# Optimization experiments

Hardware: AMD Instinct MI355X
Metric: run time of the kernel (lower is better)

## Reference

```python
import jax, jax.numpy as jnp
import numpy as np

DIST_SCALE = 10000.0   # divisor in kernel()
KERNEL_EPS = 0.0001    # additive epsilon before reciprocal


def setup_inputs() -> dict:
    key = jax.random.key(0)
    k1, k2, k3 = jax.random.split(key, 3)
    batch, keysize, dict_size, categories = 4096, 512, 16384, 128
    x = jax.random.normal(k1, (batch, keysize), dtype=jnp.float32)
    # keras TruncatedNormal(mean=0, stddev=3) approximated by scaled normal
    keys = 3.0 * jax.random.normal(k2, (dict_size, keysize), dtype=jnp.float32)
    V = jax.random.normal(k3, (dict_size, categories), dtype=jnp.float32)
    return {"x": x, "keys": keys, "V": V}


def reference(x, keys, V):
    # sq_distance(keys, x): (dict_size, batch)
    sq = (
        jnp.sum(keys * keys, axis=1, keepdims=True)            # (D, 1)
        - 2.0 * jnp.einsum("dk,bk->db", keys, x)               # (D, B)
        + jnp.sum(x * x, axis=1)[None, :]                      # (1, B)
    )
    kern = 1.0 / (sq / DIST_SCALE + KERNEL_EPS)                # (D, B)
    KV = jnp.einsum("db,dc->bc", kern, V)                      # (B, C)
    # original: diag(1 / (KV @ ones)) @ KV  ==  row-normalize by row sum
    return KV / jnp.sum(KV, axis=1, keepdims=True)
```

## Files before the change

### kernel.cpp

```cpp
#include <hip/hip_runtime.h>

#define BATCH 4096
#define DICT  16384
#define KDIM  512
#define CAT   128
#define ND    16
#define DSLICE (DICT/ND)
#define DCH   128
#define BT    256

typedef __attribute__((ext_vector_type(4))) float          f32x4;
typedef __attribute__((ext_vector_type(8))) short          short8;
typedef __attribute__((ext_vector_type(8))) unsigned short ushort8;
typedef __attribute__((ext_vector_type(4))) int            intx4;

__device__ __forceinline__ unsigned short f2bf(float f) {
  unsigned int u = __float_as_uint(f);
  return (unsigned short)((u + 0x7fffu + ((u >> 16) & 1u)) >> 16);
}

__device__ __forceinline__ unsigned int cvtpk_bf16(float lo, float hi) {
  unsigned int r;
  asm volatile("v_cvt_pk_bf16_f32 %0, %1, %2" : "=v"(r) : "v"(lo), "v"(hi));
  return r;
}

#define AS1 __attribute__((address_space(1)))
#define AS3 __attribute__((address_space(3)))
__device__ __forceinline__ void gl_lds16(const void* g, void* l) {
  __builtin_amdgcn_global_load_lds((AS1 void*)(g), (AS3 void*)(l), 16, 0, 0);
}

template <int N>
__device__ __forceinline__ void waitv() {
  if constexpr (N == 0)       asm volatile("s_waitcnt vmcnt(0)" ::: "memory");
  else if constexpr (N == 12) asm volatile("s_waitcnt vmcnt(12)" ::: "memory");
  else                        asm volatile("s_waitcnt vmcnt(14)" ::: "memory");
  __builtin_amdgcn_sched_barrier(0);
}

#define MFMA16(a, b, c) __builtin_amdgcn_mfma_f32_16x16x32_bf16((a), (b), (c), 0, 0, 0)

__global__ void prep_rows(const float* __restrict__ in,
                          unsigned short* __restrict__ ob,
                          float* __restrict__ sums) {
  const int lane = threadIdx.x & 63, wv = threadIdx.x >> 6;
  const int row = blockIdx.x * 4 + wv;
  const float* rp = in + ((size_t)row << 9);
  float4 a = *(const float4*)(rp + lane * 8);
  float4 b = *(const float4*)(rp + lane * 8 + 4);
  float s = a.x*a.x + a.y*a.y + a.z*a.z + a.w*a.w
          + b.x*b.x + b.y*b.y + b.z*b.z + b.w*b.w;
  ushort8 o;
  o[0]=f2bf(a.x); o[1]=f2bf(a.y); o[2]=f2bf(a.z); o[3]=f2bf(a.w);
  o[4]=f2bf(b.x); o[5]=f2bf(b.y); o[6]=f2bf(b.z); o[7]=f2bf(b.w);
  *(ushort8*)(ob + ((size_t)row << 9) + lane * 8) = o;
  #pragma unroll
  for (int m = 32; m; m >>= 1) s += __shfl_xor(s, m);
  if (lane == 0) sums[row] = s;
}

__global__ void prep_vt(const float* __restrict__ V,
                        unsigned short* __restrict__ Vt) {
  __shared__ float t[64][129];
  const int d0 = blockIdx.x * 64;
  const int tid = threadIdx.x;
  #pragma unroll
  for (int j = 0; j < 32; ++j) {
    int idx = j * 256 + tid;
    t[idx >> 7][idx & 127] = V[((size_t)d0 << 7) + idx];
  }
  __syncthreads();
  #pragma unroll
  for (int j = 0; j < 32; ++j) {
    int idx = j * 256 + tid;
    int cc = idx >> 6, dd = idx & 63;
    int p = dd & 31, qq = p >> 3, jj = p & 7;
    int src = (dd & 32) + 4 * qq + ((jj < 4) ? jj : (12 + jj));
    Vt[((size_t)cc << 14) + d0 + dd] = f2bf(t[src][cc]);
  }
}

__global__ __launch_bounds__(256, 1)
void varkeys_fused(const unsigned short* __restrict__ xb,
                   const unsigned short* __restrict__ kb,
                   const unsigned short* __restrict__ vt,
                   const float* __restrict__ sx,
                   const float* __restrict__ sk,
                   float* __restrict__ kvp) {
  __shared__ __attribute__((aligned(16))) char lds[131072];
  char* const VsA = lds + 98304;
  char* const VsB = lds + 114688;

  const int tid  = threadIdx.x;
  const int lane = tid & 63;
  const int wv   = tid >> 6;
  const int c    = lane & 15;
  const int h    = lane >> 4;
  const int sw   = (lane & 7) << 4;
  const int l3   = lane >> 3;

  const int bid    = blockIdx.x;
  const int btile  = bid & 15;
  const int dslice = bid >> 4;
  const int b0     = btile * BT;
  const int dbase  = dslice * DSLICE;

  float sxv[4];
  #pragma unroll
  for (int fj = 0; fj < 4; ++fj) sxv[fj] = sx[b0 + wv * 64 + fj * 16 + c];

  const int rowS = wv * 8 + l3;
  const int ofs  = (((lane & 7) ^ l3) << 4);

  const char* xbB = (const char*)xb;
  const char* kbB = (const char*)kb;
  const char* vtB = (const char*)vt;

  const f32x4 zero = {0.f, 0.f, 0.f, 0.f};
  f32x4 acc[4][8];
  #pragma unroll
  for (int j = 0; j < 4; ++j)
    #pragma unroll
    for (int n = 0; n < 8; ++n) acc[j][n] = zero;

  auto stageAB = [&](int ns) {
    const int dg2 = dbase + (ns >> 3) * DCH;
    const int kb2 = (ns & 7) << 7;
    char* A2 = lds + (ns & 1) * 16384;
    char* B2 = lds + 32768 + (ns & 1) * 32768;
    #pragma unroll
    for (int cl = 0; cl < 4; ++cl)
      gl_lds16(kbB + ((size_t)(dg2 + cl * 32 + rowS) << 10) + kb2 + ofs,
               A2 + cl * 4096 + wv * 1024);
    #pragma unroll
    for (int cl = 0; cl < 8; ++cl)
      gl_lds16(xbB + ((size_t)(b0 + cl * 32 + rowS) << 10) + kb2 + ofs,
               B2 + cl * 4096 + wv * 1024);
  };

  stageAB(0);

  f32x4 skq[8];

  for (int dc = 0; dc < DSLICE / DCH; ++dc) {
    const int dg = dbase + dc * DCH;

    f32x4 S[8][4];
    #pragma unroll
    for (int i = 0; i < 8; ++i)
      #pragma unroll
      for (int fj = 0; fj < 4; ++fj) S[i][fj] = zero;

    #pragma unroll
    for (int kk = 0; kk < 8; ++kk) {
      __builtin_amdgcn_s_barrier();
      if (kk == 0) {
        #pragma unroll
        for (int i = 0; i < 8; ++i)
          skq[i] = *(const f32x4*)(sk + dg + i * 16 + h * 4);
      }
      const int ns = dc * 8 + kk + 1;
      if (ns < 64) stageAB(ns);
      if (kk >= 2 && kk <= 5) {
        char* const VsH = (kk < 4) ? VsA : VsB;
        const int hv = (kk < 4) ? 0 : 1;
        #pragma unroll
        for (int t = 0; t < 2; ++t) {
          const int cl = ((kk - 2) & 1) * 2 + t;
          gl_lds16(vtB + ((size_t)(cl * 32 + rowS) << 15)
                       + ((size_t)(dg + hv * 64) << 1) + ofs,
                   VsH + cl * 4096 + wv * 1024);
        }
      }
      if (ns == 64) waitv<0>();
      else if (kk >= 2 && kk <= 5) waitv<14>();
      else waitv<12>();
      __builtin_amdgcn_s_barrier();
      __builtin_amdgcn_sched_barrier(0);

      const char* As = lds + (kk & 1) * 16384;
      const char* Bs = lds + 32768 + (kk & 1) * 32768;
      #pragma unroll
      for (int kf = 0; kf < 2; ++kf) {
        const int ko = (kf * 64 + h * 16) ^ sw;
        short8 bf[4];
        #pragma unroll
        for (int fj = 0; fj < 4; ++fj)
          bf[fj] = *(const short8*)(Bs + ((wv * 64 + fj * 16 + c) << 7) + ko);
        #pragma unroll
        for (int i = 0; i < 8; ++i) {
          short8 af = *(const short8*)(As + ((i * 16 + c) << 7) + ko);
          #pragma unroll
          for (int fj = 0; fj < 4; ++fj)
            S[i][fj] = MFMA16(af, bf[fj], S[i][fj]);
        }
      }
    }

    #pragma unroll
    for (int hv = 0; hv < 2; ++hv) {
      const char* VsH = hv ? VsB : VsA;
      #pragma unroll
      for (int dkh = 0; dkh < 2; ++dkh) {
        const int dk = hv * 2 + dkh;
        short8 pa[4];
        #pragma unroll
        for (int fj = 0; fj < 4; ++fj) {
          const float sv = sxv[fj];
          const f32x4 sA = S[2 * dk][fj];
          const f32x4 sB = S[2 * dk + 1][fj];
          const f32x4 kA = skq[2 * dk];
          const f32x4 kB = skq[2 * dk + 1];
          float a0 = 10000.f * __builtin_amdgcn_rcpf(kA[0] + sv - 2.f * sA[0] + 1.f);
          float a1 = 10000.f * __builtin_amdgcn_rcpf(kA[1] + sv - 2.f * sA[1] + 1.f);
          float a2 = 10000.f * __builtin_amdgcn_rcpf(kA[2] + sv - 2.f * sA[2] + 1.f);
          float a3 = 10000.f * __builtin_amdgcn_rcpf(kA[3] + sv - 2.f * sA[3] + 1.f);
          float b0f = 10000.f * __builtin_amdgcn_rcpf(kB[0] + sv - 2.f * sB[0] + 1.f);
          float b1f = 10000.f * __builtin_amdgcn_rcpf(kB[1] + sv - 2.f * sB[1] + 1.f);
          float b2f = 10000.f * __builtin_amdgcn_rcpf(kB[2] + sv - 2.f * sB[2] + 1.f);
          float b3f = 10000.f * __builtin_amdgcn_rcpf(kB[3] + sv - 2.f * sB[3] + 1.f);
          intx4 fw;
          fw[0] = (int)cvtpk_bf16(a0, a1);
          fw[1] = (int)cvtpk_bf16(a2, a3);
          fw[2] = (int)cvtpk_bf16(b0f, b1f);
          fw[3] = (int)cvtpk_bf16(b2f, b3f);
          pa[fj] = *(short8*)&fw;
        }
        const int ko = (dkh * 64 + h * 16) ^ sw;
        #pragma unroll
        for (int fc = 0; fc < 8; ++fc) {
          short8 vb = *(const short8*)(VsH + ((fc * 16 + c) << 7) + ko);
          #pragma unroll
          for (int fj = 0; fj < 4; ++fj)
            acc[fj][fc] = MFMA16(pa[fj], vb, acc[fj][fc]);
        }
      }
    }
  }

  __syncthreads();
  float* eb = (float*)(lds + (wv << 15));
  #pragma unroll
  for (int fj = 0; fj < 4; ++fj)
    #pragma unroll
    for (int r = 0; r < 4; ++r) {
      const int brow = fj * 16 + h * 4 + r;
      #pragma unroll
      for (int fc = 0; fc < 8; ++fc)
        eb[(brow << 7) + fc * 16 + c] = acc[fj][fc][r];
    }
  __syncthreads();
  float* op = kvp + (((size_t)dslice * BATCH + b0) << 7);
  const float* ebase = (const float*)lds;
  #pragma unroll
  for (int t = 0; t < 32; ++t) {
    const int row = t * 8 + (tid >> 5);
    f32x4 v = *(const f32x4*)(ebase + (row << 7) + ((tid & 31) << 2));
    *(f32x4*)(op + (((size_t)row) << 7) + ((tid & 31) << 2)) = v;
  }
}

__global__ void reduce_norm(const float* __restrict__ part, float* __restrict__ out) {
  const int lane = threadIdx.x & 63, wv = threadIdx.x >> 6;
  const int b = blockIdx.x * 4 + wv;
  float v0 = 0.f, v1 = 0.f;
  #pragma unroll
  for (int s = 0; s < ND; ++s) {
    const float* p = part + ((((size_t)s << 12) + b) << 7);
    v0 += p[lane]; v1 += p[lane + 64];
  }
  float t = v0 + v1;
  #pragma unroll
  for (int m = 32; m; m >>= 1) t += __shfl_xor(t, m);
  out[((size_t)b << 7) + lane]      = v0 / t;
  out[((size_t)b << 7) + lane + 64] = v1 / t;
}

extern "C" void kernel_launch(void* const* d_in, const int* in_sizes, int n_in,
                              void* d_out, int out_size, void* d_ws, size_t ws_size,
                              hipStream_t stream) {
  (void)in_sizes; (void)n_in; (void)out_size; (void)ws_size;
  const float* x    = (const float*)d_in[0];
  const float* keys = (const float*)d_in[1];
  const float* V    = (const float*)d_in[2];
  float* out = (float*)d_out;
  char* ws = (char*)d_ws;
  unsigned short* xb = (unsigned short*)(ws);
  unsigned short* kb = (unsigned short*)(ws + ((size_t)4 << 20));
  unsigned short* vt = (unsigned short*)(ws + ((size_t)20 << 20));
  float* sx  = (float*)(ws + ((size_t)24 << 20));
  float* sk  = (float*)(ws + ((size_t)24 << 20) + (1 << 16));
  float* kvp = (float*)(ws + ((size_t)25 << 20));

  prep_rows<<<BATCH / 4, 256, 0, stream>>>(x, xb, sx);
  prep_rows<<<DICT / 4, 256, 0, stream>>>(keys, kb, sk);
  prep_vt<<<DICT / 64, 256, 0, stream>>>(V, vt);
  varkeys_fused<<<(BATCH / BT) * ND, 256, 0, stream>>>(xb, kb, vt, sx, sk, kvp);
  reduce_norm<<<BATCH / 4, 256, 0, stream>>>(kvp, out);
}
```

Before: 157.7 us.

## Split fused kernel across 8 waves with dict-half partitioning and LDS reduction

```diff
diff --git a/kernel.cpp b/kernel.cpp
--- a/kernel.cpp
+++ b/kernel.cpp
@@ -33,9 +33,9 @@
 
 template <int N>
 __device__ __forceinline__ void waitv() {
-  if constexpr (N == 0)       asm volatile("s_waitcnt vmcnt(0)" ::: "memory");
-  else if constexpr (N == 12) asm volatile("s_waitcnt vmcnt(12)" ::: "memory");
-  else                        asm volatile("s_waitcnt vmcnt(14)" ::: "memory");
+  if constexpr (N == 0)      asm volatile("s_waitcnt vmcnt(0)" ::: "memory");
+  else if constexpr (N == 6) asm volatile("s_waitcnt vmcnt(6)" ::: "memory");
+  else                       asm volatile("s_waitcnt vmcnt(7)" ::: "memory");
   __builtin_amdgcn_sched_barrier(0);
 }
 
@@ -81,7 +81,7 @@
   }
 }
 
-__global__ __launch_bounds__(256, 1)
+__global__ __launch_bounds__(512, 2)
 void varkeys_fused(const unsigned short* __restrict__ xb,
                    const unsigned short* __restrict__ kb,
                    const unsigned short* __restrict__ vt,
@@ -95,6 +95,8 @@
   const int tid  = threadIdx.x;
   const int lane = tid & 63;
   const int wv   = tid >> 6;
+  const int dw   = wv >> 2;
+  const int bw   = wv & 3;
   const int c    = lane & 15;
   const int h    = lane >> 4;
   const int sw   = (lane & 7) << 4;
@@ -108,9 +110,9 @@
 
   float sxv[4];
   #pragma unroll
-  for (int fj = 0; fj < 4; ++fj) sxv[fj] = sx[b0 + wv * 64 + fj * 16 + c];
-
-  const int rowS = wv * 8 + l3;
+  for (int fj = 0; fj < 4; ++fj) sxv[fj] = sx[b0 + bw * 64 + fj * 16 + c];
+
+  const int rowT = wv * 8 + l3;
   const int ofs  = (((lane & 7) ^ l3) << 4);
 
   const char* xbB = (const char*)xb;
@@ -130,52 +132,49 @@
     char* A2 = lds + (ns & 1) * 16384;
     char* B2 = lds + 32768 + (ns & 1) * 32768;
     #pragma unroll
+    for (int cl = 0; cl < 2; ++cl)
+      gl_lds16(kbB + ((size_t)(dg2 + cl * 64 + rowT) << 10) + kb2 + ofs,
+               A2 + cl * 8192 + wv * 1024);
+    #pragma unroll
     for (int cl = 0; cl < 4; ++cl)
-      gl_lds16(kbB + ((size_t)(dg2 + cl * 32 + rowS) << 10) + kb2 + ofs,
-               A2 + cl * 4096 + wv * 1024);
-    #pragma unroll
-    for (int cl = 0; cl < 8; ++cl)
-      gl_lds16(xbB + ((size_t)(b0 + cl * 32 + rowS) << 10) + kb2 + ofs,
-               B2 + cl * 4096 + wv * 1024);
+      gl_lds16(xbB + ((size_t)(b0 + cl * 64 + rowT) << 10) + kb2 + ofs,
+               B2 + cl * 8192 + wv * 1024);
   };
 
   stageAB(0);
 
-  f32x4 skq[8];
+  f32x4 skq[4];
 
   for (int dc = 0; dc < DSLICE / DCH; ++dc) {
     const int dg = dbase + dc * DCH;
 
-    f32x4 S[8][4];
-    #pragma unroll
-    for (int i = 0; i < 8; ++i)
+    f32x4 S[4][4];
+    #pragma unroll
+    for (int i = 0; i < 4; ++i)
       #pragma unroll
       for (int fj = 0; fj < 4; ++fj) S[i][fj] = zero;
 
     #pragma unroll
     for (int kk = 0; kk < 8; ++kk) {
       __builtin_amdgcn_s_barrier();
-      if (kk == 0) {
-        #pragma unroll
-        for (int i = 0; i < 8; ++i)
-          skq[i] = *(const f32x4*)(sk + dg + i * 16 + h * 4);
+      if (kk == 7) {
+        #pragma unroll
+        for (int i = 0; i < 4; ++i)
+          skq[i] = *(const f32x4*)(sk + dg + dw * 64 + i * 16 + h * 4);
       }
       const int ns = dc * 8 + kk + 1;
       if (ns < 64) stageAB(ns);
       if (kk >= 2 && kk <= 5) {
         char* const VsH = (kk < 4) ? VsA : VsB;
         const int hv = (kk < 4) ? 0 : 1;
-        #pragma unroll
-        for (int t = 0; t < 2; ++t) {
-          const int cl = ((kk - 2) & 1) * 2 + t;
-          gl_lds16(vtB + ((size_t)(cl * 32 + rowS) << 15)
-                       + ((size_t)(dg + hv * 64) << 1) + ofs,
-                   VsH + cl * 4096 + wv * 1024);
-        }
+        const int vcl = kk & 1;
+        gl_lds16(vtB + ((size_t)(vcl * 64 + rowT) << 15)
+                     + ((size_t)(dg + hv * 64) << 1) + ofs,
+                 VsH + vcl * 8192 + wv * 1024);
       }
       if (ns == 64) waitv<0>();
-      else if (kk >= 2 && kk <= 5) waitv<14>();
-      else waitv<12>();
+      else if (kk >= 2 && kk <= 5) waitv<7>();
+      else waitv<6>();
       __builtin_amdgcn_s_barrier();
       __builtin_amdgcn_sched_barrier(0);
 
@@ -187,10 +186,10 @@
         short8 bf[4];
         #pragma unroll
         for (int fj = 0; fj < 4; ++fj)
-          bf[fj] = *(const short8*)(Bs + ((wv * 64 + fj * 16 + c) << 7) + ko);
-        #pragma unroll
-        for (int i = 0; i < 8; ++i) {
-          short8 af = *(const short8*)(As + ((i * 16 + c) << 7) + ko);
+          bf[fj] = *(const short8*)(Bs + ((bw * 64 + fj * 16 + c) << 7) + ko);
+        #pragma unroll
+        for (int i = 0; i < 4; ++i) {
+          short8 af = *(const short8*)(As + ((dw * 64 + i * 16 + c) << 7) + ko);
           #pragma unroll
           for (int fj = 0; fj < 4; ++fj)
             S[i][fj] = MFMA16(af, bf[fj], S[i][fj]);
@@ -198,66 +197,70 @@
       }
     }
 
-    #pragma unroll
-    for (int hv = 0; hv < 2; ++hv) {
-      const char* VsH = hv ? VsB : VsA;
-      #pragma unroll
-      for (int dkh = 0; dkh < 2; ++dkh) {
-        const int dk = hv * 2 + dkh;
-        short8 pa[4];
-        #pragma unroll
-        for (int fj = 0; fj < 4; ++fj) {
-          const float sv = sxv[fj];
-          const f32x4 sA = S[2 * dk][fj];
-          const f32x4 sB = S[2 * dk + 1][fj];
-          const f32x4 kA = skq[2 * dk];
-          const f32x4 kB = skq[2 * dk + 1];
-          float a0 = 10000.f * __builtin_amdgcn_rcpf(kA[0] + sv - 2.f * sA[0] + 1.f);
-          float a1 = 10000.f * __builtin_amdgcn_rcpf(kA[1] + sv - 2.f * sA[1] + 1.f);
-          float a2 = 10000.f * __builtin_amdgcn_rcpf(kA[2] + sv - 2.f * sA[2] + 1.f);
-          float a3 = 10000.f * __builtin_amdgcn_rcpf(kA[3] + sv - 2.f * sA[3] + 1.f);
-          float b0f = 10000.f * __builtin_amdgcn_rcpf(kB[0] + sv - 2.f * sB[0] + 1.f);
-          float b1f = 10000.f * __builtin_amdgcn_rcpf(kB[1] + sv - 2.f * sB[1] + 1.f);
-          float b2f = 10000.f * __builtin_amdgcn_rcpf(kB[2] + sv - 2.f * sB[2] + 1.f);
-          float b3f = 10000.f * __builtin_amdgcn_rcpf(kB[3] + sv - 2.f * sB[3] + 1.f);
-          intx4 fw;
-          fw[0] = (int)cvtpk_bf16(a0, a1);
-          fw[1] = (int)cvtpk_bf16(a2, a3);
-          fw[2] = (int)cvtpk_bf16(b0f, b1f);
-          fw[3] = (int)cvtpk_bf16(b2f, b3f);
-          pa[fj] = *(short8*)&fw;
-        }
-        const int ko = (dkh * 64 + h * 16) ^ sw;
-        #pragma unroll
-        for (int fc = 0; fc < 8; ++fc) {
-          short8 vb = *(const short8*)(VsH + ((fc * 16 + c) << 7) + ko);
-          #pragma unroll
-          for (int fj = 0; fj < 4; ++fj)
-            acc[fj][fc] = MFMA16(pa[fj], vb, acc[fj][fc]);
-        }
+    const char* VsH = dw ? VsB : VsA;
+    #pragma unroll
+    for (int dkh = 0; dkh < 2; ++dkh) {
+      short8 pa[4];
+      #pragma unroll
+      for (int fj = 0; fj < 4; ++fj) {
+        const float sv = sxv[fj];
+        const f32x4 sA = S[2 * dkh][fj];
+        const f32x4 sB = S[2 * dkh + 1][fj];
+        const f32x4 kA = skq[2 * dkh];
+        const f32x4 kB = skq[2 * dkh + 1];
+        float a0 = 10000.f * __builtin_amdgcn_rcpf(kA[0] + sv - 2.f * sA[0] + 1.f);
+        float a1 = 10000.f * __builtin_amdgcn_rcpf(kA[1] + sv - 2.f * sA[1] + 1.f);
+        float a2 = 10000.f * __builtin_amdgcn_rcpf(kA[2] + sv - 2.f * sA[2] + 1.f);
+        float a3 = 10000.f * __builtin_amdgcn_rcpf(kA[3] + sv - 2.f * sA[3] + 1.f);
+        float b0f = 10000.f * __builtin_amdgcn_rcpf(kB[0] + sv - 2.f * sB[0] + 1.f);
+        float b1f = 10000.f * __builtin_amdgcn_rcpf(kB[1] + sv - 2.f * sB[1] + 1.f);
+        float b2f = 10000.f * __builtin_amdgcn_rcpf(kB[2] + sv - 2.f * sB[2] + 1.f);
+        float b3f = 10000.f * __builtin_amdgcn_rcpf(kB[3] + sv - 2.f * sB[3] + 1.f);
+        intx4 fw;
+        fw[0] = (int)cvtpk_bf16(a0, a1);
+        fw[1] = (int)cvtpk_bf16(a2, a3);
+        fw[2] = (int)cvtpk_bf16(b0f, b1f);
+        fw[3] = (int)cvtpk_bf16(b2f, b3f);
+        pa[fj] = *(short8*)&fw;
+      }
+      const int ko = (dkh * 64 + h * 16) ^ sw;
+      #pragma unroll
+      for (int fc = 0; fc < 8; ++fc) {
+        short8 vb = *(const short8*)(VsH + ((fc * 16 + c) << 7) + ko);
+        #pragma unroll
+        for (int fj = 0; fj < 4; ++fj)
+          acc[fj][fc] = MFMA16(pa[fj], vb, acc[fj][fc]);
       }
     }
   }
 
   __syncthreads();
-  float* eb = (float*)(lds + (wv << 15));
-  #pragma unroll
-  for (int fj = 0; fj < 4; ++fj)
-    #pragma unroll
-    for (int r = 0; r < 4; ++r) {
-      const int brow = fj * 16 + h * 4 + r;
+  if (dw == 1) {
+    #pragma unroll
+    for (int fj = 0; fj < 4; ++fj)
       #pragma unroll
       for (int fc = 0; fc < 8; ++fc)
-        eb[(brow << 7) + fc * 16 + c] = acc[fj][fc][r];
-    }
+        *(f32x4*)(lds + bw * 32768 + (fj * 8 + fc) * 1024 + lane * 16) = acc[fj][fc];
+  }
   __syncthreads();
-  float* op = kvp + (((size_t)dslice * BATCH + b0) << 7);
-  const float* ebase = (const float*)lds;
-  #pragma unroll
-  for (int t = 0; t < 32; ++t) {
-    const int row = t * 8 + (tid >> 5);
-    f32x4 v = *(const f32x4*)(ebase + (row << 7) + ((tid & 31) << 2));
-    *(f32x4*)(op + (((size_t)row) << 7) + ((tid & 31) << 2)) = v;
+  if (dw == 0) {
+    #pragma unroll
+    for (int fj = 0; fj < 4; ++fj)
+      #pragma unroll
+      for (int fc = 0; fc < 8; ++fc) {
+        f32x4 t = *(const f32x4*)(lds + bw * 32768 + (fj * 8 + fc) * 1024 + lane * 16);
+        acc[fj][fc] += t;
+      }
+    float* op = kvp + (((size_t)(dslice * BATCH + b0 + bw * 64)) << 7);
+    #pragma unroll
+    for (int fj = 0; fj < 4; ++fj)
+      #pragma unroll
+      for (int r = 0; r < 4; ++r) {
+        const int brow = fj * 16 + h * 4 + r;
+        #pragma unroll
+        for (int fc = 0; fc < 8; ++fc)
+          op[((size_t)brow << 7) + fc * 16 + c] = acc[fj][fc][r];
+      }
   }
 }
 
@@ -296,6 +299,6 @@
   prep_rows<<<BATCH / 4, 256, 0, stream>>>(x, xb, sx);
   prep_rows<<<DICT / 4, 256, 0, stream>>>(keys, kb, sk);
   prep_vt<<<DICT / 64, 256, 0, stream>>>(V, vt);
-  varkeys_fused<<<(BATCH / BT) * ND, 256, 0, stream>>>(xb, kb, vt, sx, sk, kvp);
+  varkeys_fused<<<(BATCH / BT) * ND, 512, 0, stream>>>(xb, kb, vt, sx, sk, kvp);
   reduce_norm<<<BATCH / 4, 256, 0, stream>>>(kvp, out);
 }
```

Measured after the change: 209.7 us. 33.0% more time.
